# Performance work log

Measured on AMD Instinct MI355X. Metric: run time of the kernel, lower is better.

## Reference

```python
import math
import jax, jax.numpy as jnp
import numpy as np

# Module config (init_kwargs)
GRID = (11, 16, 24)          # (T, H, W) latent grid, T odd so T-1 == 2*(T//2)
POOL = 128                   # pool_size / block size
SPARSITY = 0.9
TXT_LEN = 384                # txt_len, txt_first=False
HEADS, HDIM = 8, 128
FFL = GRID[1] * GRID[2]      # first_frame_len = H*W = 384
SEQ = GRID[0] * FFL + TXT_LEN  # 4608 tokens, 36 blocks of 128


def _rearr(t):
    # rearrange_with_remaining, h%8==0 and w%8==0 path.
    # t: [b, (f h w), n, d] with f = T-1 frames (first frame excluded)
    b, s, n, d = t.shape
    T, H, W = GRID
    fn, hn, wn = T // 2, H // 8, W // 8
    x = t.transpose(0, 2, 1, 3).reshape(b * n, fn, 2, hn, 8, wn, 8, d)
    # 'b (fn fb)(hn hb)(wn wb) d -> b (fn hn wn fb hb wb) d'
    x = x.transpose(0, 1, 3, 5, 2, 4, 6, 7).reshape(b * n, s, d)
    return x.reshape(b, n, s, d).transpose(0, 2, 1, 3)


def _inv_rearr(t):
    b, s, n, d = t.shape
    T, H, W = GRID
    fn, hn, wn = T // 2, H // 8, W // 8
    x = t.transpose(0, 2, 1, 3).reshape(b * n, fn, hn, wn, 2, 8, 8, d)
    x = x.transpose(0, 1, 4, 2, 5, 3, 6, 7).reshape(b * n, s, d)
    return x.reshape(b, n, s, d).transpose(0, 2, 1, 3)


def _avgpool(t):
    # seq divisible by POOL -> mean over each block (tail branch unused)
    b, s, n, d = t.shape
    return t.reshape(b, s // POOL, POOL, n, d).mean(axis=2)


def _forward(q, k, v):
    b, s, n, d = q.shape
    scale = jnp.asarray(d, q.dtype) ** -0.5
    # do_tensor_rearrange_pooling on concatenated qkv (txt_first=False)
    qkv = jnp.concatenate([q, k, v], axis=0)
    f_part = qkv[:, :FFL]
    i_part = qkv[:, FFL:s - TXT_LEN]
    t_part = qkv[:, s - TXT_LEN:]
    qkv2 = jnp.concatenate([_rearr(i_part), f_part, t_part], axis=1)
    pool = _avgpool(qkv2)
    q2, k2, v2 = jnp.split(qkv2, 3, axis=0)
    qp, kp, _ = jnp.split(pool, 3, axis=0)
    # pooled block scores + softmax
    ps = jax.nn.softmax(jnp.einsum('blnd,bsnd->bnls', qp, kp) * scale, axis=-1)
    nb = s // POOL
    keep = math.ceil(nb * (1.0 - SPARSITY))
    thr = jax.lax.top_k(ps, keep)[0][..., -1:]
    mask = ps >= thr                              # [B, n, nb, nb] bool
    prot = (FFL + TXT_LEN + POOL - 1) // POOL
    mask = mask.at[:, :, -prot:, :].set(True)
    mask = mask.at[:, :, :, -prot:].set(True)
    bm = mask[0]                                  # [n, nb, nb] per-head block mask (batch 0, as kernel uses)
    tok = jnp.repeat(jnp.repeat(bm, POOL, axis=1), POOL, axis=2)  # [n, S, S]
    # block-sparse attention == masked dense attention over selected kv blocks
    scores = jnp.einsum('bqnd,bknd->bnqk', q2, k2) * scale
    scores = jnp.where(tok[None], scores, jnp.asarray(-1e30, scores.dtype))
    p = jax.nn.softmax(scores, axis=-1)
    x = jnp.einsum('bnqk,bknd->bqnd', p, v2)
    # do_tensor_inv_rearrange (txt_first=False: concat(f, i, t))
    si = s - TXT_LEN - FFL
    xi = _inv_rearr(x[:, :si])
    xf = x[:, si:si + FFL]
    xt = x[:, si + FFL:]
    return jnp.concatenate([xf, xi, xt], axis=1)


def setup_inputs() -> dict:
    key = jax.random.key(0)
    kq, kk, kv = jax.random.split(key, 3)
    q = jax.random.normal(kq, (1, SEQ, HEADS, HDIM), dtype=jnp.float32)
    k = jax.random.normal(kk, (1, SEQ, HEADS, HDIM), dtype=jnp.float32)
    v = jax.random.normal(kv, (1, SEQ, HEADS, HDIM), dtype=jnp.float32)
    t_b_idx = jnp.arange(2, dtype=jnp.int64 if jax.config.jax_enable_x64 else jnp.int32)
    return {'q': q, 'k': k, 'v': v, 't_b_idx': t_b_idx}


def reference(q, k, v, t_b_idx):
    # t_idx = t_b_idx[0] = 0, skip_timesteps = 0 -> sparse branch (static)
    return _forward(q, k, v)
```

## Files before the change

### kernel.cpp

```cpp
#include <hip/hip_runtime.h>


typedef __attribute__((ext_vector_type(8))) _Float16 half8;
typedef __attribute__((ext_vector_type(4))) _Float16 half4;
typedef __attribute__((ext_vector_type(4))) float float4v;

#define KROW 136
#define VROW 68
#define PPROW 68

__device__ __forceinline__ int orig_pos(int j) {
    if (j >= 3840) return (j < 4224) ? (j - 3840) : j;
    int blk = j >> 7;
    int r   = j & 127;
    int f   = blk / 6;
    int rem = blk - f * 6;
    int b2  = rem / 3;
    int e   = rem - b2 * 3;
    int a   = r >> 6;
    int c   = (r >> 3) & 7;
    int g   = r & 7;
    return 384 + (f * 2 + a) * 384 + (b2 * 8 + c) * 24 + e * 8 + g;
}

__device__ __forceinline__ void cp16(const void* g, void* l) {
    __builtin_amdgcn_global_load_lds((const __attribute__((address_space(1))) void*)g,
                                     (__attribute__((address_space(3))) void*)l, 16, 0, 0);
}

__global__ __launch_bounds__(256) void prep_kernel(const float* __restrict__ q,
                                                   const float* __restrict__ k,
                                                   const float* __restrict__ v,
                                                   short* __restrict__ Kc,
                                                   unsigned* __restrict__ Vt32,
                                                   float* __restrict__ qp,
                                                   float* __restrict__ kp) {
    __shared__ short Vs[64 * KROW];
    __shared__ float Rs[8 * 128];
    int bx  = blockIdx.x;
    int tid = threadIdx.x;

    if (bx < 576) {
        int sub = bx & 1;
        int kb  = (bx >> 1) % 36;
        int h   = bx / 72;

        int lr = tid >> 3;
        int ld = (tid & 7) << 2;
#pragma unroll
        for (int pass = 0; pass < 2; ++pass) {
            int lt  = pass * 32 + lr;
            int tok = sub * 64 + lt;
            int op  = orig_pos(kb * 128 + tok);
            const float* kr = k + ((size_t)op * 8 + h) * 128;
            const float* vr = v + ((size_t)op * 8 + h) * 128;
            short* ko = Kc + ((size_t)(h * 36 + kb) * 128 + tok) * KROW;
#pragma unroll
            for (int j = 0; j < 4; ++j) {
                int d = ld + j * 32;
                float4v xk = *reinterpret_cast<const float4v*>(kr + d);
                float4v xv = *reinterpret_cast<const float4v*>(vr + d);
                half4 hk, hv;
#pragma unroll
                for (int i = 0; i < 4; ++i) { hk[i] = (_Float16)xk[i]; hv[i] = (_Float16)xv[i]; }
                *reinterpret_cast<half4*>(ko + d) = hk;
                *reinterpret_cast<half4*>(&Vs[lt * KROW + d]) = hv;
            }
        }
        __syncthreads();

        {
            const unsigned short* Vsu = (const unsigned short*)Vs;
            unsigned* vo = Vt32 + (size_t)((h * 36 + kb) * 2 + sub) * 128 * (VROW / 2);
#pragma unroll
            for (int it = 0; it < 16; ++it) {
                int i   = it * 256 + tid;
                int tw  = i & 31;
                int dim = i >> 5;
                unsigned lo = Vsu[(2 * tw) * KROW + dim];
                unsigned hi = Vsu[(2 * tw + 1) * KROW + dim];
                vo[dim * (VROW / 2) + tw] = (hi << 16) | lo;
            }
        }
    } else {
        int bx2 = bx - 576;
        int sub = bx2 & 1;
        int kb  = (bx2 >> 1) % 36;
        int h   = bx2 / 72;

        const float* arr = sub ? q : k;
        int dq = (tid & 31) << 2;
        int g  = tid >> 5;
        float4v acc = {0.f, 0.f, 0.f, 0.f};
#pragma unroll
        for (int it = 0; it < 16; ++it) {
            int t  = g + it * 8;
            int op = orig_pos(kb * 128 + t);
            float4v x = *reinterpret_cast<const float4v*>(arr + ((size_t)op * 8 + h) * 128 + dq);
            acc[0] += x[0]; acc[1] += x[1]; acc[2] += x[2]; acc[3] += x[3];
        }
#pragma unroll
        for (int i = 0; i < 4; ++i) Rs[g * 128 + dq + i] = acc[i];
        __syncthreads();

        if (tid < 128) {
            float s = 0.f;
#pragma unroll
            for (int g2 = 0; g2 < 8; ++g2) s += Rs[g2 * 128 + tid];
            float* outp = sub ? qp : kp;
            outp[(h * 36 + kb) * 128 + tid] = s * (1.f / 128.f);
        }
    }
}

__global__ __launch_bounds__(128, 2) void flash_kernel(const float* __restrict__ q,
                                                       const short* __restrict__ Kc,
                                                       const short* __restrict__ Vt,
                                                       const float* __restrict__ qp,
                                                       const float* __restrict__ kp,
                                                       float* __restrict__ out,
                                                       float* __restrict__ pO,
                                                       float* __restrict__ pL) {
    __shared__ __align__(16) short Ks[64 * KROW];
    __shared__ __align__(16) short Vsh[128 * VROW];
    __shared__ __align__(16) short Ph[2 * 32 * PPROW];
    __shared__ int Ls[40];

    int t = blockIdx.x;
    int h, qb, half, nkb = 0, kbase = 0, pidx = -1;
    if (t < 288) {
        h = t & 7;
        int rest = t >> 3;
        int qbh = rest / 6, r2 = rest % 6;
        half = r2 / 3;
        int chunk = r2 % 3;
        qb = 30 + qbh; nkb = 12; kbase = chunk * 12; pidx = t;
    } else {
        int t2 = t - 288;
        h = t2 & 7;
        int rest = t2 >> 3;
        qb = rest >> 1; half = rest & 1;
    }

    int tid = threadIdx.x, wave = tid >> 6, lane = tid & 63;
    int m16 = lane & 15, quad = lane >> 4;

    constexpr float kScale = 0.08838834764831845f * 1.4426950408889634f;

    half8 aq[2][4];
#pragma unroll
    for (int rg = 0; rg < 2; ++rg) {
        int qrow_frag = qb * 128 + half * 64 + wave * 32 + rg * 16 + m16;
        const float* qrp = q + ((size_t)orig_pos(qrow_frag) * 8 + h) * 128;
#pragma unroll
        for (int kc = 0; kc < 4; ++kc) {
            float4v x0 = *reinterpret_cast<const float4v*>(qrp + kc * 32 + quad * 8);
            float4v x1 = *reinterpret_cast<const float4v*>(qrp + kc * 32 + quad * 8 + 4);
#pragma unroll
            for (int j = 0; j < 4; ++j) {
                aq[rg][kc][j]     = (_Float16)(x0[j] * kScale);
                aq[rg][kc][4 + j] = (_Float16)(x1[j] * kScale);
            }
        }
    }

    if (pidx < 0 && wave == 0) {
        float s = -1e30f;
        if (lane < 36) {
            const float4v* qv = (const float4v*)(qp + (h * 36 + qb) * 128);
            const float4v* kv = (const float4v*)(kp + (h * 36 + lane) * 128);
            float acc = 0.f;
            for (int i = 0; i < 32; ++i) {
                float4v a = qv[i], b = kv[i];
                acc += a[0] * b[0] + a[1] * b[1] + a[2] * b[2] + a[3] * b[3];
            }
            s = acc;
        }
        float tmp = s;
        float thr = 0.f;
        for (int i = 0; i < 4; ++i) {
            float mx = tmp;
            for (int off = 1; off < 64; off <<= 1) mx = fmaxf(mx, __shfl_xor(mx, off));
            thr = mx;
            unsigned long long bal = __ballot(tmp == mx);
            int low = __ffsll(bal) - 1;
            if (lane == low) tmp = -3e38f;
        }
        bool keep = (lane < 36) && ((s >= thr) || (lane >= 30));
        unsigned long long mk = __ballot(keep);
        if (lane == 0) Ls[0] = __popcll(mk);
        if (keep) {
            int pos = __popcll(mk & ((1ull << lane) - 1ull));
            Ls[1 + pos] = lane;
        }
    }
    __syncthreads();
    if (pidx < 0) nkb = Ls[0];

    float l_r[2][4];
    float4v o[2][8];
#pragma unroll
    for (int rg = 0; rg < 2; ++rg) {
#pragma unroll
        for (int r = 0; r < 4; ++r) l_r[rg][r] = 0.f;
#pragma unroll
        for (int dt = 0; dt < 8; ++dt) { o[rg][dt][0] = 0.f; o[rg][dt][1] = 0.f; o[rg][dt][2] = 0.f; o[rg][dt][3] = 0.f; }
    }

    short* Phw = Ph + wave * (32 * PPROW);

    int ntile = nkb * 2;
    for (int it = 0; it < ntile; ++it) {
        int kb  = (pidx >= 0) ? (kbase + (it >> 1)) : Ls[1 + (it >> 1)];
        int sub = it & 1;
        const char* gK = (const char*)(Kc + ((size_t)((h * 36 + kb) * 128) + sub * 64) * KROW);
        const char* gV = (const char*)(Vt + (size_t)((h * 36 + kb) * 2 + sub) * 128 * VROW);

        __syncthreads();
        {
            char* lK = (char*)Ks;
            char* lV = (char*)Vsh;
            int off = lane * 16;
            for (int c = wave; c < 34; c += 2) {
                if (c < 17) cp16(gK + c * 1024 + off, lK + c * 1024 + off);
                else        cp16(gV + (c - 17) * 1024 + off, lV + (c - 17) * 1024 + off);
            }
        }
        __syncthreads();

        float4v sacc[2][4];
#pragma unroll
        for (int rg = 0; rg < 2; ++rg)
#pragma unroll
            for (int nt = 0; nt < 4; ++nt) { sacc[rg][nt][0] = 0.f; sacc[rg][nt][1] = 0.f; sacc[rg][nt][2] = 0.f; sacc[rg][nt][3] = 0.f; }
#pragma unroll
        for (int nt = 0; nt < 4; ++nt)
#pragma unroll
            for (int kc = 0; kc < 4; ++kc) {
                half8 bk = *reinterpret_cast<const half8*>(&Ks[(nt * 16 + m16) * KROW + kc * 32 + quad * 8]);
                sacc[0][nt] = __builtin_amdgcn_mfma_f32_16x16x32_f16(aq[0][kc], bk, sacc[0][nt], 0, 0, 0);
                sacc[1][nt] = __builtin_amdgcn_mfma_f32_16x16x32_f16(aq[1][kc], bk, sacc[1][nt], 0, 0, 0);
            }

#pragma unroll
        for (int rg = 0; rg < 2; ++rg)
#pragma unroll
            for (int r = 0; r < 4; ++r) {
                float p0 = exp2f(sacc[rg][0][r]);
                float p1 = exp2f(sacc[rg][1][r]);
                float p2 = exp2f(sacc[rg][2][r]);
                float p3 = exp2f(sacc[rg][3][r]);
                sacc[rg][0][r] = p0; sacc[rg][1][r] = p1; sacc[rg][2][r] = p2; sacc[rg][3][r] = p3;
                l_r[rg][r] += (p0 + p1) + (p2 + p3);
            }

#pragma unroll
        for (int rg = 0; rg < 2; ++rg)
#pragma unroll
            for (int nt = 0; nt < 4; ++nt)
#pragma unroll
                for (int r = 0; r < 4; ++r) {
                    union { _Float16 hf; short s; } cv;
                    cv.hf = (_Float16)sacc[rg][nt][r];
                    Phw[(rg * 16 + quad * 4 + r) * PPROW + nt * 16 + m16] = cv.s;
                }
        half8 ap[2][2];
#pragma unroll
        for (int rg = 0; rg < 2; ++rg) {
            ap[rg][0] = *reinterpret_cast<const half8*>(&Phw[(rg * 16 + m16) * PPROW + quad * 8]);
            ap[rg][1] = *reinterpret_cast<const half8*>(&Phw[(rg * 16 + m16) * PPROW + 32 + quad * 8]);
        }

#pragma unroll
        for (int dt = 0; dt < 8; ++dt) {
            half8 bv0 = *reinterpret_cast<const half8*>(&Vsh[(dt * 16 + m16) * VROW + quad * 8]);
            half8 bv1 = *reinterpret_cast<const half8*>(&Vsh[(dt * 16 + m16) * VROW + 32 + quad * 8]);
#pragma unroll
            for (int rg = 0; rg < 2; ++rg) {
                float4v oc = o[rg][dt];
                oc = __builtin_amdgcn_mfma_f32_16x16x32_f16(ap[rg][0], bv0, oc, 0, 0, 0);
                oc = __builtin_amdgcn_mfma_f32_16x16x32_f16(ap[rg][1], bv1, oc, 0, 0, 0);
                o[rg][dt] = oc;
            }
        }
    }

#pragma unroll
    for (int rg = 0; rg < 2; ++rg)
#pragma unroll
        for (int r = 0; r < 4; ++r)
            for (int sh = 1; sh < 16; sh <<= 1) l_r[rg][r] += __shfl_xor(l_r[rg][r], sh);

    if (pidx >= 0) {
        float* po = pO + (size_t)pidx * 8192;
#pragma unroll
        for (int rg = 0; rg < 2; ++rg)
#pragma unroll
            for (int r = 0; r < 4; ++r) {
                int row = wave * 32 + rg * 16 + quad * 4 + r;
#pragma unroll
                for (int dt = 0; dt < 8; ++dt)
                    po[row * 128 + dt * 16 + m16] = o[rg][dt][r];
                if (m16 == 0) pL[pidx * 64 + row] = l_r[rg][r];
            }
    } else {
#pragma unroll
        for (int rg = 0; rg < 2; ++rg)
#pragma unroll
            for (int r = 0; r < 4; ++r) {
                int qrow = qb * 128 + half * 64 + wave * 32 + rg * 16 + quad * 4 + r;
                size_t base = ((size_t)orig_pos(qrow) * 8 + h) * 128;
                float inv = 1.f / l_r[rg][r];
#pragma unroll
                for (int dt = 0; dt < 8; ++dt)
                    out[base + dt * 16 + m16] = o[rg][dt][r] * inv;
            }
    }
}

__global__ void combine_kernel(const float* __restrict__ pO, const float* __restrict__ pL,
                               float* __restrict__ out) {
    int gb = blockIdx.x;
    int g  = gb >> 3;
    int rg = gb & 7;
    int h    = g / 12;
    int rem  = g % 12;
    int qbh  = rem >> 1;
    int half = rem & 1;
    int qb   = 30 + qbh;
    int base_t = (qbh * 6 + half * 3) * 8 + h;

    int tid = threadIdx.x;
    int d   = tid & 127;
    int r0  = tid >> 7;
#pragma unroll
    for (int itr = 0; itr < 4; ++itr) {
        int row = rg * 8 + r0 + itr * 2;
        float l = pL[(base_t + 0) * 64 + row] + pL[(base_t + 8) * 64 + row] + pL[(base_t + 16) * 64 + row];
        float acc = pO[(size_t)(base_t + 0) * 8192 + row * 128 + d]
                  + pO[(size_t)(base_t + 8) * 8192 + row * 128 + d]
                  + pO[(size_t)(base_t + 16) * 8192 + row * 128 + d];
        int qrow = qb * 128 + half * 64 + row;
        out[((size_t)orig_pos(qrow) * 8 + h) * 128 + d] = acc / l;
    }
}

extern "C" void kernel_launch(void* const* d_in, const int* in_sizes, int n_in,
                              void* d_out, int out_size, void* d_ws, size_t ws_size,
                              hipStream_t stream) {
    const float* q = (const float*)d_in[0];
    const float* k = (const float*)d_in[1];
    const float* v = (const float*)d_in[2];
    float* out = (float*)d_out;

    char* w = (char*)d_ws;
    short* Kc  = (short*)(w);
    short* Vt  = (short*)(w + 10027008);
    float* qp  = (float*)(w + 20054016);
    float* kp  = (float*)(w + 20201472);
    float* pL  = (float*)(w + 20348928);
    float* pO  = (float*)(w + 20422656);

    prep_kernel<<<dim3(1152), dim3(256), 0, stream>>>(q, k, v, Kc, (unsigned*)Vt, qp, kp);
    flash_kernel<<<dim3(768), dim3(128), 0, stream>>>(q, Kc, Vt, qp, kp, out, pO, pL);
    combine_kernel<<<dim3(768), dim3(256), 0, stream>>>(pO, pL, out);
}
```

Measured before the change: 196.4 us.

## Split each key tile across four waves with an LDS reduction of partial outputs

The flash kernel now runs 4 waves per block instead of 2. Each pair of waves splits the 64-key tile in half, so each wave does half the QK and PV MFMAs per tile. Partial outputs and row sums from the second key half are combined through shared memory at the end. The V row pitch grows from 68 to 72 and the P pitch shrinks, with the workspace offsets moved to match, which changes LDS bank mapping. The aim is more waves in flight to hide load and exp latency, at the cost of an extra reduction, more syncs and register pressure under the new launch bounds.

Measured after the change: 169.7 us (median of 3 runs). 1.16x faster.

```diff
diff --git a/kernel.cpp b/kernel.cpp
--- a/kernel.cpp
+++ b/kernel.cpp
@@ -6,8 +6,8 @@
 typedef __attribute__((ext_vector_type(4))) float float4v;
 
 #define KROW 136
-#define VROW 68
-#define PPROW 68
+#define VROW 72
+#define PPROW 40
 
 __device__ __forceinline__ int orig_pos(int j) {
     if (j >= 3840) return (j < 4224) ? (j - 3840) : j;
@@ -113,7 +113,7 @@
     }
 }
 
-__global__ __launch_bounds__(128, 2) void flash_kernel(const float* __restrict__ q,
+__global__ __launch_bounds__(256, 3) void flash_kernel(const float* __restrict__ q,
                                                        const short* __restrict__ Kc,
                                                        const short* __restrict__ Vt,
                                                        const float* __restrict__ qp,
@@ -123,8 +123,9 @@
                                                        float* __restrict__ pL) {
     __shared__ __align__(16) short Ks[64 * KROW];
     __shared__ __align__(16) short Vsh[128 * VROW];
-    __shared__ __align__(16) short Ph[2 * 32 * PPROW];
+    __shared__ __align__(16) short Ph[4 * 32 * PPROW];
     __shared__ int Ls[40];
+    __shared__ float Lf[64];
 
     int t = blockIdx.x;
     int h, qb, half, nkb = 0, kbase = 0, pidx = -1;
@@ -144,13 +145,14 @@
 
     int tid = threadIdx.x, wave = tid >> 6, lane = tid & 63;
     int m16 = lane & 15, quad = lane >> 4;
+    int rh = wave & 1, th = wave >> 1;
 
     constexpr float kScale = 0.08838834764831845f * 1.4426950408889634f;
 
     half8 aq[2][4];
 #pragma unroll
     for (int rg = 0; rg < 2; ++rg) {
-        int qrow_frag = qb * 128 + half * 64 + wave * 32 + rg * 16 + m16;
+        int qrow_frag = qb * 128 + half * 64 + rh * 32 + rg * 16 + m16;
         const float* qrp = q + ((size_t)orig_pos(qrow_frag) * 8 + h) * 128;
 #pragma unroll
         for (int kc = 0; kc < 4; ++kc) {
@@ -221,23 +223,23 @@
             char* lK = (char*)Ks;
             char* lV = (char*)Vsh;
             int off = lane * 16;
-            for (int c = wave; c < 34; c += 2) {
+            for (int c = wave; c < 35; c += 4) {
                 if (c < 17) cp16(gK + c * 1024 + off, lK + c * 1024 + off);
                 else        cp16(gV + (c - 17) * 1024 + off, lV + (c - 17) * 1024 + off);
             }
         }
         __syncthreads();
 
-        float4v sacc[2][4];
+        float4v sacc[2][2];
 #pragma unroll
         for (int rg = 0; rg < 2; ++rg)
 #pragma unroll
-            for (int nt = 0; nt < 4; ++nt) { sacc[rg][nt][0] = 0.f; sacc[rg][nt][1] = 0.f; sacc[rg][nt][2] = 0.f; sacc[rg][nt][3] = 0.f; }
-#pragma unroll
-        for (int nt = 0; nt < 4; ++nt)
+            for (int nt = 0; nt < 2; ++nt) { sacc[rg][nt][0] = 0.f; sacc[rg][nt][1] = 0.f; sacc[rg][nt][2] = 0.f; sacc[rg][nt][3] = 0.f; }
+#pragma unroll
+        for (int nt = 0; nt < 2; ++nt)
 #pragma unroll
             for (int kc = 0; kc < 4; ++kc) {
-                half8 bk = *reinterpret_cast<const half8*>(&Ks[(nt * 16 + m16) * KROW + kc * 32 + quad * 8]);
+                half8 bk = *reinterpret_cast<const half8*>(&Ks[(th * 32 + nt * 16 + m16) * KROW + kc * 32 + quad * 8]);
                 sacc[0][nt] = __builtin_amdgcn_mfma_f32_16x16x32_f16(aq[0][kc], bk, sacc[0][nt], 0, 0, 0);
                 sacc[1][nt] = __builtin_amdgcn_mfma_f32_16x16x32_f16(aq[1][kc], bk, sacc[1][nt], 0, 0, 0);
             }
@@ -248,40 +250,30 @@
             for (int r = 0; r < 4; ++r) {
                 float p0 = exp2f(sacc[rg][0][r]);
                 float p1 = exp2f(sacc[rg][1][r]);
-                float p2 = exp2f(sacc[rg][2][r]);
-                float p3 = exp2f(sacc[rg][3][r]);
-                sacc[rg][0][r] = p0; sacc[rg][1][r] = p1; sacc[rg][2][r] = p2; sacc[rg][3][r] = p3;
-                l_r[rg][r] += (p0 + p1) + (p2 + p3);
+                sacc[rg][0][r] = p0; sacc[rg][1][r] = p1;
+                l_r[rg][r] += p0 + p1;
             }
 
 #pragma unroll
         for (int rg = 0; rg < 2; ++rg)
 #pragma unroll
-            for (int nt = 0; nt < 4; ++nt)
+            for (int nt = 0; nt < 2; ++nt)
 #pragma unroll
                 for (int r = 0; r < 4; ++r) {
                     union { _Float16 hf; short s; } cv;
                     cv.hf = (_Float16)sacc[rg][nt][r];
                     Phw[(rg * 16 + quad * 4 + r) * PPROW + nt * 16 + m16] = cv.s;
                 }
-        half8 ap[2][2];
-#pragma unroll
-        for (int rg = 0; rg < 2; ++rg) {
-            ap[rg][0] = *reinterpret_cast<const half8*>(&Phw[(rg * 16 + m16) * PPROW + quad * 8]);
-            ap[rg][1] = *reinterpret_cast<const half8*>(&Phw[(rg * 16 + m16) * PPROW + 32 + quad * 8]);
-        }
+        half8 ap[2];
+#pragma unroll
+        for (int rg = 0; rg < 2; ++rg)
+            ap[rg] = *reinterpret_cast<const half8*>(&Phw[(rg * 16 + m16) * PPROW + quad * 8]);
 
 #pragma unroll
         for (int dt = 0; dt < 8; ++dt) {
-            half8 bv0 = *reinterpret_cast<const half8*>(&Vsh[(dt * 16 + m16) * VROW + quad * 8]);
-            half8 bv1 = *reinterpret_cast<const half8*>(&Vsh[(dt * 16 + m16) * VROW + 32 + quad * 8]);
-#pragma unroll
-            for (int rg = 0; rg < 2; ++rg) {
-                float4v oc = o[rg][dt];
-                oc = __builtin_amdgcn_mfma_f32_16x16x32_f16(ap[rg][0], bv0, oc, 0, 0, 0);
-                oc = __builtin_amdgcn_mfma_f32_16x16x32_f16(ap[rg][1], bv1, oc, 0, 0, 0);
-                o[rg][dt] = oc;
-            }
+            half8 bv = *reinterpret_cast<const half8*>(&Vsh[(dt * 16 + m16) * VROW + th * 32 + quad * 8]);
+            o[0][dt] = __builtin_amdgcn_mfma_f32_16x16x32_f16(ap[0], bv, o[0][dt], 0, 0, 0);
+            o[1][dt] = __builtin_amdgcn_mfma_f32_16x16x32_f16(ap[1], bv, o[1][dt], 0, 0, 0);
         }
     }
 
@@ -291,30 +283,61 @@
         for (int r = 0; r < 4; ++r)
             for (int sh = 1; sh < 16; sh <<= 1) l_r[rg][r] += __shfl_xor(l_r[rg][r], sh);
 
-    if (pidx >= 0) {
-        float* po = pO + (size_t)pidx * 8192;
-#pragma unroll
-        for (int rg = 0; rg < 2; ++rg)
-#pragma unroll
-            for (int r = 0; r < 4; ++r) {
-                int row = wave * 32 + rg * 16 + quad * 4 + r;
+    __syncthreads();
+    {
+        float* red = rh ? (float*)Vsh : (float*)Ks;
+        if (th == 1) {
+#pragma unroll
+            for (int rg = 0; rg < 2; ++rg) {
 #pragma unroll
                 for (int dt = 0; dt < 8; ++dt)
-                    po[row * 128 + dt * 16 + m16] = o[rg][dt][r];
-                if (m16 == 0) pL[pidx * 64 + row] = l_r[rg][r];
-            }
-    } else {
-#pragma unroll
-        for (int rg = 0; rg < 2; ++rg)
-#pragma unroll
-            for (int r = 0; r < 4; ++r) {
-                int qrow = qb * 128 + half * 64 + wave * 32 + rg * 16 + quad * 4 + r;
-                size_t base = ((size_t)orig_pos(qrow) * 8 + h) * 128;
-                float inv = 1.f / l_r[rg][r];
+#pragma unroll
+                    for (int r = 0; r < 4; ++r)
+                        red[(rg * 16 + quad * 4 + r) * 132 + dt * 16 + m16] = o[rg][dt][r];
+                if (m16 == 0)
+#pragma unroll
+                    for (int r = 0; r < 4; ++r)
+                        Lf[rh * 32 + rg * 16 + quad * 4 + r] = l_r[rg][r];
+            }
+        }
+        __syncthreads();
+        if (th == 0) {
+#pragma unroll
+            for (int rg = 0; rg < 2; ++rg)
 #pragma unroll
                 for (int dt = 0; dt < 8; ++dt)
-                    out[base + dt * 16 + m16] = o[rg][dt][r] * inv;
-            }
+#pragma unroll
+                    for (int r = 0; r < 4; ++r)
+                        o[rg][dt][r] += red[(rg * 16 + quad * 4 + r) * 132 + dt * 16 + m16];
+
+            if (pidx >= 0) {
+                float* po = pO + (size_t)pidx * 8192;
+#pragma unroll
+                for (int rg = 0; rg < 2; ++rg)
+#pragma unroll
+                    for (int r = 0; r < 4; ++r) {
+                        int row = rh * 32 + rg * 16 + quad * 4 + r;
+                        float lt2 = l_r[rg][r] + Lf[row];
+#pragma unroll
+                        for (int dt = 0; dt < 8; ++dt)
+                            po[row * 128 + dt * 16 + m16] = o[rg][dt][r];
+                        if (m16 == 0) pL[pidx * 64 + row] = lt2;
+                    }
+            } else {
+#pragma unroll
+                for (int rg = 0; rg < 2; ++rg)
+#pragma unroll
+                    for (int r = 0; r < 4; ++r) {
+                        int row = rh * 32 + rg * 16 + quad * 4 + r;
+                        int qrow = qb * 128 + half * 64 + row;
+                        size_t base = ((size_t)orig_pos(qrow) * 8 + h) * 128;
+                        float inv = 1.f / (l_r[rg][r] + Lf[row]);
+#pragma unroll
+                        for (int dt = 0; dt < 8; ++dt)
+                            out[base + dt * 16 + m16] = o[rg][dt][r] * inv;
+                    }
+            }
+        }
     }
 }
 
@@ -356,12 +379,12 @@
     char* w = (char*)d_ws;
     short* Kc  = (short*)(w);
     short* Vt  = (short*)(w + 10027008);
-    float* qp  = (float*)(w + 20054016);
-    float* kp  = (float*)(w + 20201472);
-    float* pL  = (float*)(w + 20348928);
-    float* pO  = (float*)(w + 20422656);
+    float* qp  = (float*)(w + 20643840);
+    float* kp  = (float*)(w + 20791296);
+    float* pL  = (float*)(w + 20938752);
+    float* pO  = (float*)(w + 21012480);
 
     prep_kernel<<<dim3(1152), dim3(256), 0, stream>>>(q, k, v, Kc, (unsigned*)Vt, qp, kp);
-    flash_kernel<<<dim3(768), dim3(128), 0, stream>>>(q, Kc, Vt, qp, kp, out, pO, pL);
+    flash_kernel<<<dim3(768), dim3(256), 0, stream>>>(q, Kc, Vt, qp, kp, out, pO, pL);
     combine_kernel<<<dim3(768), dim3(256), 0, stream>>>(pO, pL, out);
 }
```
